# Performance work log

Hardware: AMD Instinct MI355X
Metric: run time of the kernel (lower is better)

## Reference

```python
import jax, jax.numpy as jnp
import numpy as np

EPS = 1e-5
NUM_HEADS = 16

def rmsnorm(x, w=None, eps=EPS):
    y = x * jax.lax.rsqrt(jnp.mean(x * x, axis=-1, keepdims=True) + eps)
    return y if w is None else y * w

def act_quant(x):
    # per-token 8-bit absmax activation quantization (BitNet b1.58)
    scale = 127.0 / jnp.clip(jnp.max(jnp.abs(x), axis=-1, keepdims=True), 1e-5, None)
    return jnp.clip(jnp.round(x * scale), -128, 127) / scale

def weight_quant(w):
    # ternary (1.58-bit) absmean weight quantization
    scale = 1.0 / jnp.clip(jnp.mean(jnp.abs(w)), 1e-5, None)
    return jnp.clip(jnp.round(w * scale), -1, 1) / scale

def bit_linear(x, w):
    # BitLinear: RMSNorm -> STE-quantized activation @ STE-quantized ternary weight
    xn = rmsnorm(x)
    xq = xn + jax.lax.stop_gradient(act_quant(xn) - xn)
    wq = w + jax.lax.stop_gradient(weight_quant(w) - w)
    return xq @ wq.T

def hgrn_recurrence(i, logf):
    # elementwise gated linear recurrence: h_t = exp(logf_t) * h_{t-1} + i_t
    def step(h, xs):
        ii, ff = xs
        h = jnp.exp(ff) * h + ii
        return h, h
    B, T, D = i.shape
    _, o = jax.lax.scan(step, jnp.zeros((B, D), i.dtype),
                        (jnp.swapaxes(i, 0, 1), jnp.swapaxes(logf, 0, 1)))
    return jnp.swapaxes(o, 0, 1)  # [B, T, D]

def hgrn_bit_attention(x, w_i, w_f, w_g, w_o, g_norm_w):
    i = bit_linear(x, w_i)
    f = bit_linear(x, w_f)
    logf = jax.nn.log_sigmoid(f)
    i = jax.nn.silu(i) * (1.0 - jax.nn.sigmoid(f))  # swiglu(i, 1 - sigmoid(f))
    o = hgrn_recurrence(i, logf)
    g = bit_linear(x, w_g)
    B, T, D = o.shape
    oh = rmsnorm(o.reshape(B, T, NUM_HEADS, D // NUM_HEADS), g_norm_w)  # per-head RMSNorm
    o = oh.reshape(B, T, D) * g * jax.nn.sigmoid(g)  # swish gate (FusedRMSNormSwishGate)
    return bit_linear(o, w_o)

def setup_inputs() -> dict:
    key = jax.random.key(0)
    B, S_S, S_C, D = 4, 4096, 512, 2048
    ks = jax.random.split(key, 16)
    mk = lambda k: jax.random.normal(k, (D, D), jnp.float32) * 0.02
    return {
        "hidden_states": jax.random.normal(ks[0], (B, S_S, D), jnp.float32),
        "encoder_hidden_states": jax.random.normal(ks[1], (B, S_C, D), jnp.float32),
        "w_q": mk(ks[2]), "w_k": mk(ks[3]), "w_v": mk(ks[4]), "w_out": mk(ks[5]),
        "w_add_q": mk(ks[6]), "w_add_k": mk(ks[7]), "w_add_v": mk(ks[8]), "w_add_out": mk(ks[9]),
        "w_i": mk(ks[10]), "w_f": mk(ks[11]), "w_g": mk(ks[12]), "w_o": mk(ks[13]),
        "g_norm_w": jnp.ones((D // NUM_HEADS,), jnp.float32),
    }

def reference(hidden_states, encoder_hidden_states, w_q, w_k, w_v, w_out,
              w_add_q, w_add_k, w_add_v, w_add_out, w_i, w_f, w_g, w_o, g_norm_w):
    q_s = bit_linear(hidden_states, w_q)
    k_s = bit_linear(hidden_states, w_k)          # computed as in original; unused by attn
    v_s = bit_linear(hidden_states, w_v)          # computed as in original; unused by attn
    q_c = bit_linear(encoder_hidden_states, w_add_q)
    k_c = bit_linear(encoder_hidden_states, w_add_k)
    v_c = bit_linear(encoder_hidden_states, w_add_v)
    q_joint = jnp.concatenate([q_c, q_s], axis=1)  # context first, then stream
    attn_out = hgrn_bit_attention(q_joint, w_i, w_f, w_g, w_o, g_norm_w)
    len_c = encoder_hidden_states.shape[1]
    out_c, out_s = attn_out[:, :len_c, :], attn_out[:, len_c:, :]
    return (bit_linear(out_s, w_out), bit_linear(out_c, w_add_out))
```

## Files before the change

kernel.cpp:

```cpp
#include <hip/hip_runtime.h>
#include <math.h>
#include <stdint.h>

#define D2 2048

typedef int v4i __attribute__((ext_vector_type(4)));
typedef int v16i __attribute__((ext_vector_type(16)));

struct Ptrs8 { const float* p[8]; };
struct RowMap { int seg, jump, off; };

enum { QW_Q = 0, QW_OUT = 1, QW_ADDQ = 2, QW_ADDOUT = 3, QW_I = 4, QW_F = 5, QW_G = 6, QW_O = 7 };

__device__ __forceinline__ int rmap(RowMap m, int r) {
  return (r / m.seg) * m.jump + (r % m.seg) + m.off;
}

__device__ __forceinline__ void gload16(const void* g, void* l) {
  __builtin_amdgcn_global_load_lds((__attribute__((address_space(1))) void*)g,
                                   (__attribute__((address_space(3))) void*)l, 16, 0, 0);
}

__device__ __forceinline__ float fsig(float x) {
  return __builtin_amdgcn_rcpf(1.0f + __expf(-x));
}

template <bool NT>
__device__ __forceinline__ void stf(float* p, float v) {
  if (NT) __builtin_nontemporal_store(v, p);
  else *p = v;
}

__device__ __forceinline__ int swz(int r) { return ((r >> 1) & 3) ^ ((r >> 3) & 3); }

__device__ __forceinline__ void gswz16(int nM, int& mb, int& nb) {
  int bid = blockIdx.x;
  int wg = (bid & 7) * (nM << 1) + (bid >> 3);
  mb = wg >> 4;
  nb = wg & 15;
}
__device__ __forceinline__ void gswz8(int nM, int& mb, int& nb) {
  int bid = blockIdx.x;
  int wg = (bid & 7) * nM + (bid >> 3);
  mb = wg >> 3;
  nb = wg & 7;
}

__global__ __launch_bounds__(256) void k_wabs(Ptrs8 wsrc, double* part) {
  int m = blockIdx.y;
  const float4* w4 = (const float4*)(wsrc.p[m] + (size_t)blockIdx.x * 4096 + threadIdx.x * 16);
  double s = 0.0;
#pragma unroll
  for (int j = 0; j < 4; ++j) {
    float4 v = w4[j];
    s += (double)fabsf(v.x) + (double)fabsf(v.y) + (double)fabsf(v.z) + (double)fabsf(v.w);
  }
#pragma unroll
  for (int o = 32; o; o >>= 1) s += __shfl_down(s, o);
  __shared__ double red[4];
  if ((threadIdx.x & 63) == 0) red[threadIdx.x >> 6] = s;
  __syncthreads();
  if (threadIdx.x == 0) part[(size_t)m * 1024 + blockIdx.x] = red[0] + red[1] + red[2] + red[3];
}

__global__ __launch_bounds__(256) void k_wmean(const double* part, double* wqs, float* wmul) {
  int m = blockIdx.x, t = threadIdx.x;
  const double* p = part + (size_t)m * 1024;
  double s = p[t] + p[t + 256] + p[t + 512] + p[t + 768];
#pragma unroll
  for (int o = 32; o; o >>= 1) s += __shfl_down(s, o);
  __shared__ double red[4];
  if ((t & 63) == 0) red[t >> 6] = s;
  __syncthreads();
  if (t == 0) {
    double mean = (red[0] + red[1] + red[2] + red[3]) * (1.0 / 4194304.0);
    double cl = mean > 1e-5 ? mean : 1e-5;
    wqs[m] = 1.0 / cl;
    wmul[m] = (float)cl;
  }
}

__global__ __launch_bounds__(256) void k_wquant(Ptrs8 wsrc, const double* wqs, int8_t* wq) {
  int m = blockIdx.y;
  double qs = wqs[m];
  size_t base = (size_t)blockIdx.x * 4096 + threadIdx.x * 16;
  const float4* w4 = (const float4*)(wsrc.p[m] + base);
  union { int8_t b[16]; int4 v; } u;
#pragma unroll
  for (int j = 0; j < 4; ++j) {
    float4 v = w4[j];
    float f[4] = {v.x, v.y, v.z, v.w};
#pragma unroll
    for (int c = 0; c < 4; ++c) {
      int q = (int)rint((double)f[c] * qs);
      q = q > 1 ? 1 : (q < -1 ? -1 : q);
      u.b[j * 4 + c] = (int8_t)q;
    }
  }
  *(int4*)(wq + (size_t)m * 4194304 + base) = u.v;
}

__global__ __launch_bounds__(256) void k_actq(const float* __restrict__ x, int8_t* __restrict__ q,
                                              float* __restrict__ inv) {
  int row = blockIdx.x, t = threadIdx.x;
  const float4* xr = (const float4*)(x + (size_t)row * D2);
  float4 a = xr[t * 2], b = xr[t * 2 + 1];
  float v[8] = {a.x, a.y, a.z, a.w, b.x, b.y, b.z, b.w};
  float ss = 0.f, ma = 0.f;
#pragma unroll
  for (int j = 0; j < 8; ++j) { ss += v[j] * v[j]; ma = fmaxf(ma, fabsf(v[j])); }
#pragma unroll
  for (int o = 32; o; o >>= 1) { ss += __shfl_down(ss, o); ma = fmaxf(ma, __shfl_down(ma, o)); }
  __shared__ float rs[4], rm[4], bc[2];
  if ((t & 63) == 0) { rs[t >> 6] = ss; rm[t >> 6] = ma; }
  __syncthreads();
  if (t == 0) {
    float S = rs[0] + rs[1] + rs[2] + rs[3];
    float M = fmaxf(fmaxf(rm[0], rm[1]), fmaxf(rm[2], rm[3]));
    float r = 1.0f / sqrtf(S * (1.0f / 2048.0f) + 1e-5f);
    float mx = fmaxf(M * r, 1e-5f);
    bc[0] = r;
    bc[1] = 127.0f / mx;
    inv[row] = mx * (1.0f / 127.0f);
  }
  __syncthreads();
  float r = bc[0], s = bc[1];
  union { int8_t b8[8]; int2 p2; } u;
#pragma unroll
  for (int j = 0; j < 8; ++j) {
    float xn = v[j] * r;
    int qq = (int)rintf(xn * s);
    qq = qq > 127 ? 127 : (qq < -128 ? -128 : qq);
    u.b8[j] = (int8_t)qq;
  }
  ((int2*)(q + (size_t)row * D2))[t] = u.p2;
}

#define SYNC_PIPE(N)                                          \
  do {                                                        \
    __builtin_amdgcn_sched_barrier(0);                        \
    asm volatile("s_waitcnt vmcnt(" #N ")" ::: "memory");     \
    __builtin_amdgcn_sched_barrier(0);                        \
    __builtin_amdgcn_s_barrier();                             \
    __builtin_amdgcn_sched_barrier(0);                        \
  } while (0)

__device__ __forceinline__ void gemm_mainloop(const int8_t* __restrict__ Aq,
                                              const int8_t* __restrict__ Wq, int ga0, int ga1,
                                              int n0, int t, int8_t* lds, v16i acc[2][4]) {
  const int wid = t >> 6, lane = t & 63;
  const int wr = wid >> 1, wc = wid & 1, am = lane & 31, g = lane >> 5;
  const int arow = t >> 2;
  const int achk = ((t & 3) ^ swz(arow)) * 16;
  const int8_t* agp0 = Aq + (size_t)ga0 * 2048 + achk;
  const int8_t* agp1 = Aq + (size_t)ga1 * 2048 + achk;
  const int8_t* bgp0 = Wq + (size_t)(n0 + arow) * 2048 + achk;
  const int8_t* bgp1 = Wq + (size_t)(n0 + 64 + arow) * 2048 + achk;
  const int8_t* bgp2 = Wq + (size_t)(n0 + 128 + arow) * 2048 + achk;
  const int8_t* bgp3 = Wq + (size_t)(n0 + 192 + arow) * 2048 + achk;

#define STAGEW(B)                                                \
  do {                                                           \
    gload16(agp0, lds + (B) + wid * 1024);                       \
    gload16(agp1, lds + (B) + 4096 + wid * 1024);                \
    gload16(bgp0, lds + (B) + 8192 + wid * 1024);                \
    gload16(bgp1, lds + (B) + 12288 + wid * 1024);               \
    gload16(bgp2, lds + (B) + 16384 + wid * 1024);               \
    gload16(bgp3, lds + (B) + 20480 + wid * 1024);               \
    agp0 += 64; agp1 += 64;                                      \
    bgp0 += 64; bgp1 += 64; bgp2 += 64; bgp3 += 64;              \
  } while (0)

#define COMPUTEW(B)                                                                         \
  do {                                                                                      \
    _Pragma("unroll") for (int kk = 0; kk < 2; ++kk) {                                      \
      v4i af[2], bf[4];                                                                     \
      _Pragma("unroll") for (int mi = 0; mi < 2; ++mi) {                                    \
        int r = wr * 64 + mi * 32 + am;                                                     \
        int slot = ((kk << 1) | g) ^ swz(r);                                                \
        af[mi] = *(const v4i*)(lds + (B) + r * 64 + slot * 16);                             \
      }                                                                                     \
      _Pragma("unroll") for (int ni = 0; ni < 4; ++ni) {                                    \
        int rb = wc * 128 + ni * 32 + am;                                                   \
        int slotb = ((kk << 1) | g) ^ swz(rb);                                              \
        bf[ni] = *(const v4i*)(lds + (B) + 8192 + rb * 64 + slotb * 16);                    \
      }                                                                                     \
      _Pragma("unroll") for (int mi = 0; mi < 2; ++mi)                                      \
        _Pragma("unroll") for (int ni = 0; ni < 4; ++ni)                                    \
          acc[mi][ni] =                                                                     \
              __builtin_amdgcn_mfma_i32_32x32x32_i8(af[mi], bf[ni], acc[mi][ni], 0, 0, 0);  \
    }                                                                                       \
  } while (0)

  STAGEW(0);
  STAGEW(24576);
  STAGEW(49152);
  SYNC_PIPE(12);
#pragma unroll 1
  for (int tt = 0; tt < 30; tt += 3) {
    COMPUTEW(0);
    SYNC_PIPE(6);
    if (tt + 3 < 32) STAGEW(0);
    COMPUTEW(24576);
    SYNC_PIPE(6);
    if (tt + 4 < 32) STAGEW(24576);
    COMPUTEW(49152);
    SYNC_PIPE(6);
    if (tt + 5 < 32) STAGEW(49152);
  }
  COMPUTEW(0);
  SYNC_PIPE(0);
  COMPUTEW(24576);
#undef STAGEW
#undef COMPUTEW
}

template <bool NT>
__device__ __forceinline__ void gemm_body(const int8_t* Aq, const float* ainv, const int8_t* Wq,
                                          const float* wmul, int widx, float* C, RowMap inm,
                                          RowMap outm, int m0, int n0, int t, int8_t* lds) {
  int lane = t & 63, wid = t >> 6;
  int wr = wid >> 1, wc = wid & 1;
  int am = lane & 31, g = lane >> 5;
  int ga0 = rmap(inm, m0 + (t >> 2));
  int ga1 = rmap(inm, m0 + 64 + (t >> 2));

  v16i acc[2][4] = {};
  gemm_mainloop(Aq, Wq, ga0, ga1, n0, t, lds, acc);

  float wm = wmul[widx];
#pragma unroll
  for (int mi = 0; mi < 2; ++mi) {
#pragma unroll
    for (int q = 0; q < 16; ++q) {
      int rin = wr * 64 + mi * 32 + (q & 3) + ((q >> 2) * 8) + g * 4;
      int ra = rmap(inm, m0 + rin);
      int rc = rmap(outm, m0 + rin);
      float s = ainv[ra] * wm;
#pragma unroll
      for (int ni = 0; ni < 4; ++ni) {
        stf<NT>(&C[(size_t)rc * 2048 + n0 + wc * 128 + ni * 32 + am], (float)acc[mi][ni][q] * s);
      }
    }
  }
}

template <bool NT>
__global__ __launch_bounds__(256) void k_gemm(const int8_t* __restrict__ Aq,
                                              const float* __restrict__ ainv,
                                              const int8_t* __restrict__ Wq,
                                              const float* __restrict__ wmul, int widx,
                                              float* __restrict__ C, RowMap inm, RowMap outm,
                                              int nM) {
  __shared__ __align__(16) int8_t lds[73728];
  int mb, nb;
  gswz8(nM, mb, nb);
  gemm_body<NT>(Aq, ainv, Wq, wmul, widx, C, inm, outm, mb * 128, nb * 256, threadIdx.x, lds);
}

template <bool NT>
__global__ __launch_bounds__(256) void k_gemm2(const int8_t* __restrict__ Aq,
                                               const float* __restrict__ ainv,
                                               const int8_t* __restrict__ W0, int w0idx,
                                               RowMap inm0, RowMap outm0, float* __restrict__ C0,
                                               int nM0,
                                               const int8_t* __restrict__ W1, int w1idx,
                                               RowMap inm1, RowMap outm1, float* __restrict__ C1,
                                               int nM1, const float* __restrict__ wmul) {
  __shared__ __align__(16) int8_t lds[73728];
  int mb, nb;
  gswz8(nM0 + nM1, mb, nb);
  if (mb < nM0) {
    gemm_body<NT>(Aq, ainv, W0, wmul, w0idx, C0, inm0, outm0, mb * 128, nb * 256, threadIdx.x,
                  lds);
  } else {
    gemm_body<NT>(Aq, ainv, W1, wmul, w1idx, C1, inm1, outm1, (mb - nM0) * 128, nb * 256,
                  threadIdx.x, lds);
  }
}

__global__ __launch_bounds__(256) void k_gemm_if(const int8_t* __restrict__ Aq,
                                                 const float* __restrict__ ainv,
                                                 const int8_t* __restrict__ Wi,
                                                 const int8_t* __restrict__ Wf,
                                                 const float* __restrict__ wmul,
                                                 float* __restrict__ IG, float* __restrict__ AD,
                                                 int nM) {
  __shared__ __align__(16) int8_t lds[73728];
  int mb, nb;
  gswz16(nM, mb, nb);
  int m0 = mb * 128, n0 = nb * 128;
  int t = threadIdx.x;
  const int wid = t >> 6, lane = t & 63;
  const int wr = wid >> 1, wc = wid & 1, am = lane & 31, g = lane >> 5;
  const int arow = t >> 2;
  const int achk = ((t & 3) ^ swz(arow)) * 16;
  const int8_t* agp0 = Aq + (size_t)(m0 + arow) * 2048 + achk;
  const int8_t* agp1 = Aq + (size_t)(m0 + 64 + arow) * 2048 + achk;
  const int8_t* bip0 = Wi + (size_t)(n0 + arow) * 2048 + achk;
  const int8_t* bip1 = Wi + (size_t)(n0 + 64 + arow) * 2048 + achk;
  const int8_t* bfp0 = Wf + (size_t)(n0 + arow) * 2048 + achk;
  const int8_t* bfp1 = Wf + (size_t)(n0 + 64 + arow) * 2048 + achk;

  v16i acci[2][2] = {};
  v16i accf[2][2] = {};

#define STAGE_IF(B)                                                                   \
  do {                                                                                \
    gload16(agp0, lds + (B) + wid * 1024);                                            \
    gload16(agp1, lds + (B) + 4096 + wid * 1024);                                     \
    gload16(bip0, lds + (B) + 8192 + wid * 1024);                                     \
    gload16(bip1, lds + (B) + 12288 + wid * 1024);                                    \
    gload16(bfp0, lds + (B) + 16384 + wid * 1024);                                    \
    gload16(bfp1, lds + (B) + 20480 + wid * 1024);                                    \
    agp0 += 64; agp1 += 64; bip0 += 64; bip1 += 64; bfp0 += 64; bfp1 += 64;           \
  } while (0)

#define COMPUTE_IF(B)                                                                       \
  do {                                                                                      \
    _Pragma("unroll") for (int kk = 0; kk < 2; ++kk) {                                      \
      v4i af[2], bfi[2], bff[2];                                                            \
      _Pragma("unroll") for (int mi = 0; mi < 2; ++mi) {                                    \
        int r = wr * 64 + mi * 32 + am;                                                     \
        int slot = ((kk << 1) | g) ^ swz(r);                                                \
        af[mi] = *(const v4i*)(lds + (B) + r * 64 + slot * 16);                             \
      }                                                                                     \
      _Pragma("unroll") for (int ni = 0; ni < 2; ++ni) {                                    \
        int rb = wc * 64 + ni * 32 + am;                                                    \
        int slotb = ((kk << 1) | g) ^ swz(rb);                                              \
        bfi[ni] = *(const v4i*)(lds + (B) + 8192 + rb * 64 + slotb * 16);                   \
        bff[ni] = *(const v4i*)(lds + (B) + 16384 + rb * 64 + slotb * 16);                  \
      }                                                                                     \
      _Pragma("unroll") for (int mi = 0; mi < 2; ++mi)                                      \
        _Pragma("unroll") for (int ni = 0; ni < 2; ++ni) {                                  \
          acci[mi][ni] =                                                                    \
              __builtin_amdgcn_mfma_i32_32x32x32_i8(af[mi], bfi[ni], acci[mi][ni], 0, 0, 0);\
          accf[mi][ni] =                                                                    \
              __builtin_amdgcn_mfma_i32_32x32x32_i8(af[mi], bff[ni], accf[mi][ni], 0, 0, 0);\
        }                                                                                   \
    }                                                                                       \
  } while (0)

  STAGE_IF(0);
  STAGE_IF(24576);
  STAGE_IF(49152);
  SYNC_PIPE(12);
#pragma unroll 1
  for (int tt = 0; tt < 30; tt += 3) {
    COMPUTE_IF(0);
    SYNC_PIPE(6);
    if (tt + 3 < 32) STAGE_IF(0);
    COMPUTE_IF(24576);
    SYNC_PIPE(6);
    if (tt + 4 < 32) STAGE_IF(24576);
    COMPUTE_IF(49152);
    SYNC_PIPE(6);
    if (tt + 5 < 32) STAGE_IF(49152);
  }
  COMPUTE_IF(0);
  SYNC_PIPE(0);
  COMPUTE_IF(24576);
#undef STAGE_IF
#undef COMPUTE_IF

  float wmi = wmul[QW_I], wmf = wmul[QW_F];
#pragma unroll
  for (int mi = 0; mi < 2; ++mi) {
#pragma unroll
    for (int q = 0; q < 16; ++q) {
      int rin = m0 + wr * 64 + mi * 32 + (q & 3) + ((q >> 2) * 8) + g * 4;
      float si = ainv[rin] * wmi;
      float sf = ainv[rin] * wmf;
#pragma unroll
      for (int ni = 0; ni < 2; ++ni) {
        size_t idx = (size_t)rin * 2048 + n0 + wc * 64 + ni * 32 + am;
        float iv = (float)acci[mi][ni][q] * si;
        float fv = (float)accf[mi][ni][q] * sf;
        float a = fsig(fv);
        float s2 = iv * fsig(iv);
        __builtin_nontemporal_store(s2 * (1.0f - a), &IG[idx]);
        __builtin_nontemporal_store(a, &AD[idx]);
      }
    }
  }
}

__global__ __launch_bounds__(256) void k_rec1(const float* __restrict__ ig,
                                              const float* __restrict__ ad,
                                              float* __restrict__ chA, float* __restrict__ chH) {
  int tid = blockIdx.x * 256 + threadIdx.x;
  int chain = tid & 8191;
  int c = tid >> 13;
  int b = chain >> 11, d = chain & 2047;
  size_t base = ((size_t)b * 4608 + (size_t)c * 72) * 2048 + d;
  float h = 0.f, P = 1.f;
  for (int s = 0; s < 72; ++s) {
    float av = ad[base];
    float iv = __builtin_nontemporal_load(ig + base);
    h = av * h + iv;
    P *= av;
    base += 2048;
  }
  chA[(size_t)c * 8192 + chain] = P;
  chH[(size_t)c * 8192 + chain] = h;
}

__global__ __launch_bounds__(256) void k_rec2(const float* __restrict__ chA,
                                              const float* __restrict__ chH,
                                              float* __restrict__ chC) {
  int chain = blockIdx.x * 256 + threadIdx.x;
  float carry = 0.f;
  for (int c = 0; c < 64; ++c) {
    chC[(size_t)c * 8192 + chain] = carry;
    carry = chA[(size_t)c * 8192 + chain] * carry + chH[(size_t)c * 8192 + chain];
  }
}

__global__ __launch_bounds__(256) void k_rec3(float* __restrict__ io, const float* __restrict__ ad,
                                              const float* __restrict__ chC) {
  int tid = blockIdx.x * 256 + threadIdx.x;
  int chain = tid & 8191;
  int c = tid >> 13;
  int b = chain >> 11, d = chain & 2047;
  size_t base = ((size_t)b * 4608 + (size_t)c * 72) * 2048 + d;
  float h = chC[(size_t)c * 8192 + chain];
  for (int s = 0; s < 72; ++s) {
    float av = ad[base];
    float iv = io[base];
    h = av * h + iv;
    io[base] = h;
    base += 2048;
  }
}

__global__ __launch_bounds__(256) void k_hnq(const float* __restrict__ o,
                                             const float* __restrict__ g,
                                             const float* __restrict__ gnw,
                                             int8_t* __restrict__ q, float* __restrict__ inv) {
  int row = blockIdx.x, t = threadIdx.x;
  size_t base = (size_t)row * D2 + (size_t)t * 8;
  float4 a = *(const float4*)(o + base);
  float4 b = *(const float4*)(o + base + 4);
  float v[8] = {a.x, a.y, a.z, a.w, b.x, b.y, b.z, b.w};
  float ss = 0.f;
#pragma unroll
  for (int j = 0; j < 8; ++j) ss += v[j] * v[j];
  ss += __shfl_xor(ss, 1);
  ss += __shfl_xor(ss, 2);
  ss += __shfl_xor(ss, 4);
  ss += __shfl_xor(ss, 8);
  float r = 1.0f / sqrtf(ss * (1.0f / 128.0f) + 1e-5f);
  float4 ga = *(const float4*)(g + base);
  float4 gb = *(const float4*)(g + base + 4);
  float gv[8] = {ga.x, ga.y, ga.z, ga.w, gb.x, gb.y, gb.z, gb.w};
  int j0 = (t & 15) * 8;
  float o2[8];
#pragma unroll
  for (int j = 0; j < 8; ++j) {
    float gg = gv[j];
    o2[j] = v[j] * r * gnw[j0 + j] * gg * fsig(gg);
  }
  float ss2 = 0.f, ma = 0.f;
#pragma unroll
  for (int j = 0; j < 8; ++j) { ss2 += o2[j] * o2[j]; ma = fmaxf(ma, fabsf(o2[j])); }
#pragma unroll
  for (int off = 32; off; off >>= 1) {
    ss2 += __shfl_down(ss2, off);
    ma = fmaxf(ma, __shfl_down(ma, off));
  }
  __shared__ float rs[4], rm[4], bc[2];
  if ((t & 63) == 0) { rs[t >> 6] = ss2; rm[t >> 6] = ma; }
  __syncthreads();
  if (t == 0) {
    float S = rs[0] + rs[1] + rs[2] + rs[3];
    float M = fmaxf(fmaxf(rm[0], rm[1]), fmaxf(rm[2], rm[3]));
    float rr = 1.0f / sqrtf(S * (1.0f / 2048.0f) + 1e-5f);
    float mx = fmaxf(M * rr, 1e-5f);
    bc[0] = rr;
    bc[1] = 127.0f / mx;
    inv[row] = mx * (1.0f / 127.0f);
  }
  __syncthreads();
  float rr = bc[0], s = bc[1];
  union { int8_t b8[8]; int2 p2; } u;
#pragma unroll
  for (int j = 0; j < 8; ++j) {
    float xn = o2[j] * rr;
    int qq = (int)rintf(xn * s);
    qq = qq > 127 ? 127 : (qq < -128 ? -128 : qq);
    u.b8[j] = (int8_t)qq;
  }
  ((int2*)(q + (size_t)row * D2))[t] = u.p2;
}

extern "C" void kernel_launch(void* const* d_in, const int* in_sizes, int n_in,
                              void* d_out, int out_size, void* d_ws, size_t ws_size,
                              hipStream_t stream) {
  const float* hid = (const float*)d_in[0];
  const float* enc = (const float*)d_in[1];
  const float* gnw = (const float*)d_in[14];
  Ptrs8 wp;
  wp.p[QW_Q] = (const float*)d_in[2];
  wp.p[QW_OUT] = (const float*)d_in[5];
  wp.p[QW_ADDQ] = (const float*)d_in[6];
  wp.p[QW_ADDOUT] = (const float*)d_in[9];
  wp.p[QW_I] = (const float*)d_in[10];
  wp.p[QW_F] = (const float*)d_in[11];
  wp.p[QW_G] = (const float*)d_in[12];
  wp.p[QW_O] = (const float*)d_in[13];
  float* out = (float*)d_out;

  char* ws = (char*)d_ws;
  float* bufA = (float*)ws;
  float* bufB = bufA + 37748736;
  int8_t* actq = (int8_t*)(bufB + 37748736);
  int8_t* wq = actq + 37748736;
  float* ainv = (float*)(wq + 33554432);
  double* wpart = (double*)(ainv + 18432);
  double* wqs = wpart + 8192;
  float* wmul = (float*)(wqs + 8);
  float* chA = wmul + 8;
  float* chH = chA + 524288;
  float* chC = chH + 524288;
  if (ws_size < 379723872ULL) return;

  RowMap idm{0x40000000, 0, 0};
  RowMap encoff{0x40000000, 0, 16384};
  RowMap seqm{4096, 4608, 512};
  RowMap encm{512, 4608, 0};

  k_wabs<<<dim3(1024, 8), 256, 0, stream>>>(wp, wpart);
  k_wmean<<<8, 256, 0, stream>>>(wpart, wqs, wmul);
  k_wquant<<<dim3(1024, 8), 256, 0, stream>>>(wp, wqs, wq);
  k_actq<<<16384, 256, 0, stream>>>(hid, actq, ainv);
  k_actq<<<2048, 256, 0, stream>>>(enc, actq + (size_t)16384 * 2048, ainv + 16384);
  k_gemm2<false><<<(128 + 16) * 8, 256, 0, stream>>>(
      actq, ainv, wq + (size_t)QW_Q * 4194304, QW_Q, idm, seqm, bufA, 128,
      wq + (size_t)QW_ADDQ * 4194304, QW_ADDQ, encoff, encm, bufA, 16, wmul);
  k_actq<<<18432, 256, 0, stream>>>(bufA, actq, ainv);
  k_gemm_if<<<144 * 16, 256, 0, stream>>>(actq, ainv, wq + (size_t)QW_I * 4194304,
                                          wq + (size_t)QW_F * 4194304, wmul, bufA, bufB, 144);
  k_gemm<true><<<144 * 8, 256, 0, stream>>>(actq, ainv, wq + (size_t)QW_G * 4194304, wmul,
                                            QW_G, out, idm, idm, 144);
  k_rec1<<<2048, 256, 0, stream>>>(bufA, bufB, chA, chH);
  k_rec2<<<32, 256, 0, stream>>>(chA, chH, chC);
  k_rec3<<<2048, 256, 0, stream>>>(bufA, bufB, chC);
  k_hnq<<<18432, 256, 0, stream>>>(bufA, out, gnw, actq, ainv);
  k_gemm<false><<<144 * 8, 256, 0, stream>>>(actq, ainv, wq + (size_t)QW_O * 4194304, wmul,
                                             QW_O, bufB, idm, idm, 144);
  k_actq<<<18432, 256, 0, stream>>>(bufB, actq, ainv);
  k_gemm2<true><<<(128 + 16) * 8, 256, 0, stream>>>(
      actq, ainv, wq + (size_t)QW_OUT * 4194304, QW_OUT, seqm, idm, out, 128,
      wq + (size_t)QW_ADDOUT * 4194304, QW_ADDOUT, encm, idm, out + (size_t)33554432, 16, wmul);
}
```

Measured before the change: 965.0 us.

## Fuse chunk-level recurrence summaries into i/f GEMM epilogue, drop rec1 pass

New measurement: 920.7 us. 4.6% less time.

```diff
diff --git a/kernel.cpp b/kernel.cpp
--- a/kernel.cpp
+++ b/kernel.cpp
@@ -6,6 +6,7 @@
 
 typedef int v4i __attribute__((ext_vector_type(4)));
 typedef int v16i __attribute__((ext_vector_type(16)));
+typedef float v4f __attribute__((ext_vector_type(4)));
 
 struct Ptrs8 { const float* p[8]; };
 struct RowMap { int seg, jump, off; };
@@ -29,6 +30,10 @@
 __device__ __forceinline__ void stf(float* p, float v) {
   if (NT) __builtin_nontemporal_store(v, p);
   else *p = v;
+}
+
+__device__ __forceinline__ v4f ldnt4(const float* p) {
+  return __builtin_nontemporal_load((const v4f*)p);
 }
 
 __device__ __forceinline__ int swz(int r) { return ((r >> 1) & 3) ^ ((r >> 3) & 3); }
@@ -48,12 +53,12 @@
 
 __global__ __launch_bounds__(256) void k_wabs(Ptrs8 wsrc, double* part) {
   int m = blockIdx.y;
-  const float4* w4 = (const float4*)(wsrc.p[m] + (size_t)blockIdx.x * 4096 + threadIdx.x * 16);
+  const float* w0 = wsrc.p[m] + (size_t)blockIdx.x * 4096 + threadIdx.x * 16;
   double s = 0.0;
 #pragma unroll
   for (int j = 0; j < 4; ++j) {
-    float4 v = w4[j];
-    s += (double)fabsf(v.x) + (double)fabsf(v.y) + (double)fabsf(v.z) + (double)fabsf(v.w);
+    v4f v = ldnt4(w0 + j * 4);
+    s += (double)fabsf(v[0]) + (double)fabsf(v[1]) + (double)fabsf(v[2]) + (double)fabsf(v[3]);
   }
 #pragma unroll
   for (int o = 32; o; o >>= 1) s += __shfl_down(s, o);
@@ -84,15 +89,14 @@
   int m = blockIdx.y;
   double qs = wqs[m];
   size_t base = (size_t)blockIdx.x * 4096 + threadIdx.x * 16;
-  const float4* w4 = (const float4*)(wsrc.p[m] + base);
+  const float* w0 = wsrc.p[m] + base;
   union { int8_t b[16]; int4 v; } u;
 #pragma unroll
   for (int j = 0; j < 4; ++j) {
-    float4 v = w4[j];
-    float f[4] = {v.x, v.y, v.z, v.w};
+    v4f v = ldnt4(w0 + j * 4);
 #pragma unroll
     for (int c = 0; c < 4; ++c) {
-      int q = (int)rint((double)f[c] * qs);
+      int q = (int)rint((double)v[c] * qs);
       q = q > 1 ? 1 : (q < -1 ? -1 : q);
       u.b[j * 4 + c] = (int8_t)q;
     }
@@ -103,9 +107,10 @@
 __global__ __launch_bounds__(256) void k_actq(const float* __restrict__ x, int8_t* __restrict__ q,
                                               float* __restrict__ inv) {
   int row = blockIdx.x, t = threadIdx.x;
-  const float4* xr = (const float4*)(x + (size_t)row * D2);
-  float4 a = xr[t * 2], b = xr[t * 2 + 1];
-  float v[8] = {a.x, a.y, a.z, a.w, b.x, b.y, b.z, b.w};
+  const float* xr = x + (size_t)row * D2 + (size_t)t * 8;
+  v4f a = ldnt4(xr);
+  v4f b = ldnt4(xr + 4);
+  float v[8] = {a[0], a[1], a[2], a[3], b[0], b[1], b[2], b[3]};
   float ss = 0.f, ma = 0.f;
 #pragma unroll
   for (int j = 0; j < 8; ++j) { ss += v[j] * v[j]; ma = fmaxf(ma, fabsf(v[j])); }
@@ -285,6 +290,7 @@
                                                  const int8_t* __restrict__ Wf,
                                                  const float* __restrict__ wmul,
                                                  float* __restrict__ IG, float* __restrict__ AD,
+                                                 float* __restrict__ chA, float* __restrict__ chH,
                                                  int nM) {
   __shared__ __align__(16) int8_t lds[73728];
   int mb, nb;
@@ -364,45 +370,59 @@
 #undef COMPUTE_IF
 
   float wmi = wmul[QW_I], wmf = wmul[QW_F];
+  __syncthreads();
+  float2* seglds = (float2*)lds;
 #pragma unroll
   for (int mi = 0; mi < 2; ++mi) {
 #pragma unroll
-    for (int q = 0; q < 16; ++q) {
-      int rin = m0 + wr * 64 + mi * 32 + (q & 3) + ((q >> 2) * 8) + g * 4;
-      float si = ainv[rin] * wmi;
-      float sf = ainv[rin] * wmf;
-#pragma unroll
-      for (int ni = 0; ni < 2; ++ni) {
-        size_t idx = (size_t)rin * 2048 + n0 + wc * 64 + ni * 32 + am;
-        float iv = (float)acci[mi][ni][q] * si;
-        float fv = (float)accf[mi][ni][q] * sf;
-        float a = fsig(fv);
-        float s2 = iv * fsig(iv);
-        __builtin_nontemporal_store(s2 * (1.0f - a), &IG[idx]);
-        __builtin_nontemporal_store(a, &AD[idx]);
+    for (int qh = 0; qh < 4; ++qh) {
+      float segP[2], segH[2];
+#pragma unroll
+      for (int ql = 0; ql < 4; ++ql) {
+        int q = qh * 4 + ql;
+        int rloc = wr * 64 + mi * 32 + qh * 8 + g * 4 + ql;
+        int rin = m0 + rloc;
+        float ai = ainv[rin];
+        float si = ai * wmi, sf = ai * wmf;
+#pragma unroll
+        for (int ni = 0; ni < 2; ++ni) {
+          size_t idx = (size_t)rin * 2048 + n0 + wc * 64 + ni * 32 + am;
+          float iv = (float)acci[mi][ni][q] * si;
+          float fv = (float)accf[mi][ni][q] * sf;
+          float a = fsig(fv);
+          float s2 = iv * fsig(iv);
+          float igv = s2 * (1.0f - a);
+          __builtin_nontemporal_store(igv, &IG[idx]);
+          __builtin_nontemporal_store(a, &AD[idx]);
+          if (ql == 0) {
+            segP[ni] = a;
+            segH[ni] = igv;
+          } else {
+            segH[ni] = a * segH[ni] + igv;
+            segP[ni] *= a;
+          }
+        }
       }
+      int seg = wr * 16 + mi * 8 + qh * 2 + g;
+#pragma unroll
+      for (int ni = 0; ni < 2; ++ni)
+        seglds[seg * 128 + wc * 64 + ni * 32 + am] = make_float2(segP[ni], segH[ni]);
     }
   }
-}
-
-__global__ __launch_bounds__(256) void k_rec1(const float* __restrict__ ig,
-                                              const float* __restrict__ ad,
-                                              float* __restrict__ chA, float* __restrict__ chH) {
-  int tid = blockIdx.x * 256 + threadIdx.x;
-  int chain = tid & 8191;
-  int c = tid >> 13;
-  int b = chain >> 11, d = chain & 2047;
-  size_t base = ((size_t)b * 4608 + (size_t)c * 72) * 2048 + d;
-  float h = 0.f, P = 1.f;
-  for (int s = 0; s < 72; ++s) {
-    float av = ad[base];
-    float iv = __builtin_nontemporal_load(ig + base);
-    h = av * h + iv;
-    P *= av;
-    base += 2048;
-  }
-  chA[(size_t)c * 8192 + chain] = P;
-  chH[(size_t)c * 8192 + chain] = h;
+  __syncthreads();
+  if (t < 128) {
+    float P = 1.f, H = 0.f;
+#pragma unroll 1
+    for (int s = 0; s < 32; ++s) {
+      float2 e = seglds[s * 128 + t];
+      H = e.x * H + e.y;
+      P *= e.x;
+    }
+    int bb = mb / 36, ck = mb - bb * 36;
+    int chain = bb * 2048 + n0 + t;
+    chA[(size_t)ck * 8192 + chain] = P;
+    chH[(size_t)ck * 8192 + chain] = H;
+  }
 }
 
 __global__ __launch_bounds__(256) void k_rec2(const float* __restrict__ chA,
@@ -410,7 +430,7 @@
                                               float* __restrict__ chC) {
   int chain = blockIdx.x * 256 + threadIdx.x;
   float carry = 0.f;
-  for (int c = 0; c < 64; ++c) {
+  for (int c = 0; c < 36; ++c) {
     chC[(size_t)c * 8192 + chain] = carry;
     carry = chA[(size_t)c * 8192 + chain] * carry + chH[(size_t)c * 8192 + chain];
   }
@@ -422,10 +442,10 @@
   int chain = tid & 8191;
   int c = tid >> 13;
   int b = chain >> 11, d = chain & 2047;
-  size_t base = ((size_t)b * 4608 + (size_t)c * 72) * 2048 + d;
+  size_t base = ((size_t)b * 4608 + (size_t)c * 128) * 2048 + d;
   float h = chC[(size_t)c * 8192 + chain];
-  for (int s = 0; s < 72; ++s) {
-    float av = ad[base];
+  for (int s = 0; s < 128; ++s) {
+    float av = __builtin_nontemporal_load(ad + base);
     float iv = io[base];
     h = av * h + iv;
     io[base] = h;
@@ -439,9 +459,9 @@
                                              int8_t* __restrict__ q, float* __restrict__ inv) {
   int row = blockIdx.x, t = threadIdx.x;
   size_t base = (size_t)row * D2 + (size_t)t * 8;
-  float4 a = *(const float4*)(o + base);
-  float4 b = *(const float4*)(o + base + 4);
-  float v[8] = {a.x, a.y, a.z, a.w, b.x, b.y, b.z, b.w};
+  v4f a = ldnt4(o + base);
+  v4f b = ldnt4(o + base + 4);
+  float v[8] = {a[0], a[1], a[2], a[3], b[0], b[1], b[2], b[3]};
   float ss = 0.f;
 #pragma unroll
   for (int j = 0; j < 8; ++j) ss += v[j] * v[j];
@@ -450,9 +470,9 @@
   ss += __shfl_xor(ss, 4);
   ss += __shfl_xor(ss, 8);
   float r = 1.0f / sqrtf(ss * (1.0f / 128.0f) + 1e-5f);
-  float4 ga = *(const float4*)(g + base);
-  float4 gb = *(const float4*)(g + base + 4);
-  float gv[8] = {ga.x, ga.y, ga.z, ga.w, gb.x, gb.y, gb.z, gb.w};
+  v4f ga = ldnt4(g + base);
+  v4f gb = ldnt4(g + base + 4);
+  float gv[8] = {ga[0], ga[1], ga[2], ga[3], gb[0], gb[1], gb[2], gb[3]};
   int j0 = (t & 15) * 8;
   float o2[8];
 #pragma unroll
@@ -539,12 +559,12 @@
       wq + (size_t)QW_ADDQ * 4194304, QW_ADDQ, encoff, encm, bufA, 16, wmul);
   k_actq<<<18432, 256, 0, stream>>>(bufA, actq, ainv);
   k_gemm_if<<<144 * 16, 256, 0, stream>>>(actq, ainv, wq + (size_t)QW_I * 4194304,
-                                          wq + (size_t)QW_F * 4194304, wmul, bufA, bufB, 144);
+                                          wq + (size_t)QW_F * 4194304, wmul, bufA, bufB,
+                                          chA, chH, 144);
   k_gemm<true><<<144 * 8, 256, 0, stream>>>(actq, ainv, wq + (size_t)QW_G * 4194304, wmul,
                                             QW_G, out, idm, idm, 144);
-  k_rec1<<<2048, 256, 0, stream>>>(bufA, bufB, chA, chH);
   k_rec2<<<32, 256, 0, stream>>>(chA, chH, chC);
-  k_rec3<<<2048, 256, 0, stream>>>(bufA, bufB, chC);
+  k_rec3<<<1152, 256, 0, stream>>>(bufA, bufB, chC);
   k_hnq<<<18432, 256, 0, stream>>>(bufA, out, gnw, actq, ainv);
   k_gemm<false><<<144 * 8, 256, 0, stream>>>(actq, ainv, wq + (size_t)QW_O * 4194304, wmul,
                                              QW_O, bufB, idm, idm, 144);
```
